# Optimization experiments

Hardware: AMD Instinct MI355X
Metric: run time of the kernel (lower is better)

Reference implementation:

```python
import jax, jax.numpy as jnp
import numpy as np

CH = 512
HEADS = 4
GROUPS = 32  # _groups(512) -> 32
EPS = 1e-5


def setup_inputs() -> dict:
    key = jax.random.key(0)
    ks = jax.random.split(key, 7)
    b, c, h, w = 16, CH, 32, 32
    sd = 1.0 / np.sqrt(c)
    return {
        "x": jax.random.normal(ks[0], (b, c, h, w), dtype=jnp.float32),
        "gamma": jnp.ones((c,), jnp.float32),
        "beta": jnp.zeros((c,), jnp.float32),
        "w_qkv": jax.random.normal(ks[1], (3 * c, c), dtype=jnp.float32) * sd,
        "b_qkv": jax.random.normal(ks[2], (3 * c,), dtype=jnp.float32) * 0.01,
        "w_proj": jax.random.normal(ks[3], (c, c), dtype=jnp.float32) * sd,
        "b_proj": jax.random.normal(ks[4], (c,), dtype=jnp.float32) * 0.01,
    }


def _group_norm(x, gamma, beta):
    b, c, h, w = x.shape
    xg = x.reshape(b, GROUPS, -1)  # (b, G, c//G * h * w)
    mu = jnp.mean(xg, axis=-1, keepdims=True)
    var = jnp.var(xg, axis=-1, keepdims=True)
    xn = ((xg - mu) * jax.lax.rsqrt(var + EPS)).reshape(b, c, h, w)
    return xn * gamma[None, :, None, None] + beta[None, :, None, None]


def reference(x, gamma, beta, w_qkv, b_qkv, w_proj, b_proj):
    b, c, h, w = x.shape
    hd = c // HEADS
    xn = _group_norm(x, gamma, beta)
    # 1x1 conv == channel matmul
    qkv = jnp.einsum('oc,bchw->bohw', w_qkv, xn) + b_qkv[None, :, None, None]
    qkv = qkv.reshape(b, 3, HEADS, hd, h * w)
    q, k, v = qkv[:, 0], qkv[:, 1], qkv[:, 2]  # (b, H, hd, n)
    scale = hd ** -0.5
    attn = jax.nn.softmax(jnp.einsum('bhcn,bhcm->bhnm', q * scale, k), axis=-1)
    out = jnp.einsum('bhnm,bhcm->bhcn', attn, v).reshape(b, c, h, w)
    out = jnp.einsum('oc,bchw->bohw', w_proj, out) + b_proj[None, :, None, None]
    return x + out
```

## Files before the change

### kernel.cpp

```cpp
#include <hip/hip_runtime.h>

#define CH 512
#define HEADS 4
#define HD 128
#define NPIX 1024
#define BATCH 16
#define GROUPS 32
#define GSZ 16
#define EPS 1e-5f

typedef _Float16 f16;
typedef _Float16 f16x8 __attribute__((ext_vector_type(8)));
typedef _Float16 f16x4 __attribute__((ext_vector_type(4)));
typedef float f32x4 __attribute__((ext_vector_type(4)));

__device__ __forceinline__ void gld16(const f16* g, f16* l) {
    __builtin_amdgcn_global_load_lds((__attribute__((address_space(1))) const void*)g,
                                     (__attribute__((address_space(3))) void*)l, 16, 0, 0);
}

__global__ __launch_bounds__(256, 2) void k_pre(const float* __restrict__ x, const float* __restrict__ gamma,
                                                const float* __restrict__ beta, f16* __restrict__ xnT,
                                                const float* __restrict__ wq, const float* __restrict__ wp,
                                                f16* __restrict__ wqT, f16* __restrict__ wpT) {
    __shared__ float xs[GSZ * NPIX];
    __shared__ float red[8];
    __shared__ float stat2[2];
    int bidx = blockIdx.x;
    if (bidx >= 512) {
        int c = (bidx - 512) * 256 + threadIdx.x;
        {
            int ot = c >> 13, kbl = (c >> 7) & 63, ol = c & 127;
            const float* s = wq + ((size_t)(ot * 128 + ol)) * CH + kbl * 8;
            f32x4 a = *(const f32x4*)s, b2 = *(const f32x4*)(s + 4);
            f16x8 v;
            v[0] = (f16)a.x; v[1] = (f16)a.y; v[2] = (f16)a.z; v[3] = (f16)a.w;
            v[4] = (f16)b2.x; v[5] = (f16)b2.y; v[6] = (f16)b2.z; v[7] = (f16)b2.w;
            *(f16x8*)(wqT + (size_t)c * 8) = v;
        }
        if (c < 32768) {
            int ot = c >> 13, kbl = (c >> 7) & 63, ol = c & 127;
            const float* s = wp + ((size_t)(ot * 128 + ol)) * CH + kbl * 8;
            f32x4 a = *(const f32x4*)s, b2 = *(const f32x4*)(s + 4);
            f16x8 v;
            v[0] = (f16)a.x; v[1] = (f16)a.y; v[2] = (f16)a.z; v[3] = (f16)a.w;
            v[4] = (f16)b2.x; v[5] = (f16)b2.y; v[6] = (f16)b2.z; v[7] = (f16)b2.w;
            *(f16x8*)(wpT + (size_t)c * 8) = v;
        }
        return;
    }
    int g = bidx & 31, b = bidx >> 5;
    const f32x4* x4 = (const f32x4*)(x + ((size_t)(b * GROUPS + g)) * (GSZ * NPIX));
    float s = 0.f, ss = 0.f;
    for (int i = threadIdx.x; i < GSZ * NPIX / 4; i += 256) {
        f32x4 v = x4[i];
        *(f32x4*)&xs[i * 4] = v;
        s  += v.x + v.y + v.z + v.w;
        ss += v.x * v.x + v.y * v.y + v.z * v.z + v.w * v.w;
    }
    for (int off = 32; off; off >>= 1) { s += __shfl_down(s, off); ss += __shfl_down(ss, off); }
    int wv = threadIdx.x >> 6, ln = threadIdx.x & 63;
    if (ln == 0) { red[wv] = s; red[4 + wv] = ss; }
    __syncthreads();
    if (threadIdx.x == 0) {
        float S = red[0] + red[1] + red[2] + red[3];
        float SS = red[4] + red[5] + red[6] + red[7];
        float mu = S / (GSZ * NPIX);
        float var = SS / (GSZ * NPIX) - mu * mu;
        stat2[0] = mu; stat2[1] = rsqrtf(var + EPS);
    }
    __syncthreads();
    float mu = stat2[0], rstd = stat2[1];
    int ch = threadIdx.x >> 7;
    int n  = threadIdx.x & 127;
    float gl[8], bl[8];
#pragma unroll
    for (int i = 0; i < 8; i++) {
        float gv = gamma[g * 16 + ch * 8 + i] * rstd;
        gl[i] = gv;
        bl[i] = beta[g * 16 + ch * 8 + i] - mu * gv;
    }
    f16* tb0 = xnT + ((size_t)(b * 8)) * 65536 + (g * 2 + ch) * 1024 + n * 8;
#pragma unroll
    for (int nt = 0; nt < 8; nt++) {
        f16x8 o;
#pragma unroll
        for (int i = 0; i < 8; i++)
            o[i] = (f16)(xs[(ch * 8 + i) * 1024 + nt * 128 + n] * gl[i] + bl[i]);
        *(f16x8*)(tb0 + (size_t)nt * 65536) = o;
    }
}

__global__ __launch_bounds__(256, 3) void k_qkv(const f16* __restrict__ wT, const float* __restrict__ bias,
                                                const f16* __restrict__ xnT, f16* __restrict__ qF,
                                                f16* __restrict__ kTl, f16* __restrict__ vTl) {
    int nt = blockIdx.x, ot = blockIdx.y, b = blockIdx.z;
    int o0 = ot * 128;
    __shared__ union SM {
        struct { f16 As[8192]; f16 Bs[8192]; } s;
        f16 Cf[16384];
    } sm;
    __shared__ float biasS[128];
    if (threadIdx.x < 128) biasS[threadIdx.x] = bias[o0 + threadIdx.x];
    int tid = threadIdx.x, lane = tid & 63, wv = tid >> 6;
    int wr = wv >> 1, wc = wv & 1;
    int l15 = lane & 15, quad = lane >> 4;
    const f16* wA = wT + (size_t)ot * 65536;
    const f16* xB = xnT + ((size_t)(b * 8 + nt)) * 65536;
    f32x4 acc[4][4] = {};
    for (int kk = 0; kk < CH; kk += 64) {
        __syncthreads();
        const f16* sa = wA + (size_t)(kk >> 3) * 1024;
        const f16* sb = xB + (size_t)(kk >> 3) * 1024;
#pragma unroll
        for (int i = 0; i < 4; i++) {
            int s = wv * 4 + i;
            gld16(sa + (size_t)(s * 64 + lane) * 8, sm.s.As + s * 512);
            gld16(sb + (size_t)(s * 64 + lane) * 8, sm.s.Bs + s * 512);
        }
        __syncthreads();
#pragma unroll
        for (int dk = 0; dk < 2; dk++) {
            f16x8 af[4], bf[4];
#pragma unroll
            for (int t = 0; t < 4; t++) {
                af[t] = *(const f16x8*)(sm.s.As + (dk * 4 + quad) * 1024 + (wr * 64 + t * 16 + l15) * 8);
                bf[t] = *(const f16x8*)(sm.s.Bs + (dk * 4 + quad) * 1024 + (wc * 64 + t * 16 + l15) * 8);
            }
#pragma unroll
            for (int tm = 0; tm < 4; tm++)
#pragma unroll
                for (int tn = 0; tn < 4; tn++)
                    acc[tm][tn] = __builtin_amdgcn_mfma_f32_16x16x32_f16(af[tm], bf[tn], acc[tm][tn], 0, 0, 0);
        }
    }
    __syncthreads();
    int which = ot >> 2, h = ot & 3;
#pragma unroll
    for (int tm = 0; tm < 4; tm++)
#pragma unroll
        for (int tn = 0; tn < 4; tn++) {
            int ob = wr * 64 + tm * 16 + quad * 4;
            int n  = wc * 64 + tn * 16 + l15;
            f16x4 pv;
#pragma unroll
            for (int r = 0; r < 4; r++) pv[r] = (f16)(acc[tm][tn][r] + biasS[ob + r]);
            if (which == 0) {
                int addr = ((((n >> 5) * 2 + ((n >> 4) & 1)) * 4 + (ob >> 5)) * 512)
                         + ((ob >> 3) & 3) * 128 + (n & 15) * 8 + (quad & 1) * 4;
                *(f16x4*)&sm.Cf[addr] = pv;
            } else if (which == 1) {
                int addr = (ob >> 3) * 1024 + n * 8 + (quad & 1) * 4;
                *(f16x4*)&sm.Cf[addr] = pv;
            } else {
#pragma unroll
                for (int r = 0; r < 4; r++)
                    sm.Cf[(n >> 3) * 1024 + (ob + r) * 8 + (n & 7)] = pv[r];
            }
        }
    __syncthreads();
    f16* tb = (which == 0) ? (qF + ((size_t)((b * 4 + h) * 8 + nt)) * 16384)
            : (which == 1) ? (kTl + ((size_t)((b * 4 + h) * 8 + nt)) * 16384)
                           : (vTl + ((size_t)((b * 4 + h) * 8 + nt)) * 16384);
#pragma unroll
    for (int i = 0; i < 8; i++) {
        int cid = tid + i * 256;
        *(f16x8*)(tb + (size_t)cid * 8) = *(const f16x8*)(sm.Cf + cid * 8);
    }
}

__global__ __launch_bounds__(512, 4) void k_attn(const f16* __restrict__ qF, const f16* __restrict__ kTl,
                                                 const f16* __restrict__ vTl, f16* __restrict__ oT) {
    __shared__ f16 smem[16384];
    f16* Kl = smem;
    f16* Vl = smem + 8192;
    int bid = blockIdx.x;
    int nt = bid >> 6, group = bid & 63;
    int b = group >> 2, h = group & 3;
    int tid = threadIdx.x, lane = tid & 63, wv = tid >> 6;
    int wq = wv & 3, role = wv >> 2;
    int l15 = lane & 15, quad = lane >> 4;
    const f16* qb = qF + ((size_t)(group * 8 + nt)) * 16384;
    const f16* kb = kTl + (size_t)group * 8 * 16384;
    const f16* vb = vTl + (size_t)group * 8 * 16384;
    f16* dstL = role ? Vl : Kl;

    f16x8 aq[4];
#pragma unroll
    for (int dk = 0; dk < 4; dk++) {
        f16x8 v = *(const f16x8*)(qb + (wv * 4 + dk) * 512 + lane * 8);
        aq[dk] = v * (f16)(0.08838834764831845f * 1.4426950408889634f);
    }

    float m_i = -1e30f, l_i = 0.f;
    f32x4 oaccT[8] = {};

    f16x8 buf[4];
    if (role == 0) {
#pragma unroll
        for (int i = 0; i < 4; i++)
            buf[i] = *(const f16x8*)(kb + (size_t)(wq * 4 + i) * 1024 + lane * 8);
    } else {
#pragma unroll
        for (int i = 0; i < 4; i++)
            buf[i] = *(const f16x8*)(vb + (size_t)(wq * 4 + i) * 512 + lane * 8);
    }

    for (int mc = 0; mc < 16; mc++) {
        __syncthreads();
#pragma unroll
        for (int i = 0; i < 4; i++)
            *(f16x8*)&dstL[(wq * 4 + i) * 512 + lane * 8] = buf[i];
        __syncthreads();

        f32x4 st[4] = {};
#pragma unroll
        for (int dk = 0; dk < 4; dk++) {
            f16x8 kf[4];
#pragma unroll
            for (int t = 0; t < 4; t++)
                kf[t] = *(const f16x8*)&Kl[(dk * 4 + quad) * 512 + (t * 16 + l15) * 8];
#pragma unroll
            for (int tc = 0; tc < 4; tc++)
                st[tc] = __builtin_amdgcn_mfma_f32_16x16x32_f16(kf[tc], aq[dk], st[tc], 0, 0, 0);
        }

        float a[4];
#pragma unroll
        for (int tc = 0; tc < 4; tc++)
            a[tc] = fmaxf(fmaxf(st[tc][0], st[tc][1]), fmaxf(st[tc][2], st[tc][3]));
        a[0] = fmaxf(a[0], a[2]); a[1] = fmaxf(a[1], a[3]);
        float mx = fmaxf(a[0], a[1]);
        mx = fmaxf(mx, __shfl_xor(mx, 16));
        mx = fmaxf(mx, __shfl_xor(mx, 32));

        bool full = !__all(mx <= m_i + 8.f);
        float mnew = m_i, alpha = 1.f;
        if (full) {
            mnew = fmaxf(m_i, mx);
            alpha = __builtin_amdgcn_exp2f(m_i - mnew);
            m_i = mnew;
        }

        float r4[4];
#pragma unroll
        for (int tc = 0; tc < 4; tc++) {
            float p0 = __builtin_amdgcn_exp2f(st[tc][0] - mnew);
            float p1 = __builtin_amdgcn_exp2f(st[tc][1] - mnew);
            float p2 = __builtin_amdgcn_exp2f(st[tc][2] - mnew);
            float p3 = __builtin_amdgcn_exp2f(st[tc][3] - mnew);
            st[tc][0] = p0; st[tc][1] = p1;
            st[tc][2] = p2; st[tc][3] = p3;
            r4[tc] = (p0 + p1) + (p2 + p3);
        }
        float rs = (r4[0] + r4[1]) + (r4[2] + r4[3]);
        rs += __shfl_xor(rs, 16);
        rs += __shfl_xor(rs, 32);
        if (full) {
            l_i = l_i * alpha + rs;
#pragma unroll
            for (int tc = 0; tc < 8; tc++) {
                oaccT[tc].x *= alpha; oaccT[tc].y *= alpha;
                oaccT[tc].z *= alpha; oaccT[tc].w *= alpha;
            }
        } else {
            l_i += rs;
        }

        f16x4 pf[4];
#pragma unroll
        for (int tc = 0; tc < 4; tc++)
#pragma unroll
            for (int r = 0; r < 4; r++) pf[tc][r] = (f16)st[tc][r];

        if (mc < 15) {
            if (role == 0) {
                const f16* s = kb + (size_t)((mc + 1) >> 1) * 16384 + (size_t)((mc + 1) & 1) * 512;
#pragma unroll
                for (int i = 0; i < 4; i++)
                    buf[i] = *(const f16x8*)(s + (size_t)(wq * 4 + i) * 1024 + lane * 8);
            } else {
                const f16* s = vb + (size_t)(mc + 1) * 8192;
#pragma unroll
                for (int i = 0; i < 4; i++)
                    buf[i] = *(const f16x8*)(s + (size_t)(wq * 4 + i) * 512 + lane * 8);
            }
        }

#pragma unroll
        for (int kblk = 0; kblk < 4; kblk++) {
#pragma unroll
            for (int t = 0; t < 8; t++) {
                f16x4 vf = *(const f16x4*)&Vl[(kblk * 2 + (quad >> 1)) * 1024 + (t * 16 + l15) * 8 + (quad & 1) * 4];
                oaccT[t] = __builtin_amdgcn_mfma_f32_16x16x16f16(vf, pf[kblk], oaccT[t], 0, 0, 0);
            }
        }
    }

    __syncthreads();
    {
        float inv = 1.f / l_i;
        int n = wv * 16 + l15;
#pragma unroll
        for (int tc = 0; tc < 8; tc++) {
            int blk = tc * 2 + (quad >> 1);
            f16x4 ov;
#pragma unroll
            for (int r = 0; r < 4; r++) ov[r] = (f16)(oaccT[tc][r] * inv);
            *(f16x4*)&smem[n * 128 + ((blk ^ (n & 15)) << 3) + ((quad & 1) << 2)] = ov;
        }
    }
    __syncthreads();
    f16* ob = oT + ((size_t)(b * 8 + nt)) * 65536;
#pragma unroll
    for (int i = 0; i < 4; i++) {
        int cid = tid + i * 512;
        int cbl = cid >> 7, n = cid & 127;
        f16x8 v = *(const f16x8*)&smem[n * 128 + ((cbl ^ (n & 15)) << 3)];
        *(f16x8*)(ob + (size_t)(h * 16 + cbl) * 1024 + n * 8) = v;
    }
}

__global__ __launch_bounds__(256, 3) void k_proj(const f16* __restrict__ wT, const float* __restrict__ bias,
                                                 const f16* __restrict__ oT, const float* __restrict__ x,
                                                 float* __restrict__ out) {
    int nt = blockIdx.x, ot = blockIdx.y, b = blockIdx.z;
    int n0 = nt * 128, o0 = ot * 128;
    __shared__ union SM {
        struct { f16 As[8192]; f16 Bs[8192]; } s;
        f16 Cs[128][136];
    } sm;
    __shared__ float biasS[128];
    if (threadIdx.x < 128) biasS[threadIdx.x] = bias[o0 + threadIdx.x];
    int tid = threadIdx.x, lane = tid & 63, wv = tid >> 6;
    int wr = wv >> 1, wc = wv & 1;
    int l15 = lane & 15, quad = lane >> 4;
    const f16* wA = wT + (size_t)ot * 65536;
    const f16* xB = oT + ((size_t)(b * 8 + nt)) * 65536;
    f32x4 acc[4][4] = {};
    for (int kk = 0; kk < CH; kk += 64) {
        __syncthreads();
        const f16* sa = wA + (size_t)(kk >> 3) * 1024;
        const f16* sb = xB + (size_t)(kk >> 3) * 1024;
#pragma unroll
        for (int i = 0; i < 4; i++) {
            int s = wv * 4 + i;
            gld16(sa + (size_t)(s * 64 + lane) * 8, sm.s.As + s * 512);
            gld16(sb + (size_t)(s * 64 + lane) * 8, sm.s.Bs + s * 512);
        }
        __syncthreads();
#pragma unroll
        for (int dk = 0; dk < 2; dk++) {
            f16x8 af[4], bf[4];
#pragma unroll
            for (int t = 0; t < 4; t++) {
                af[t] = *(const f16x8*)(sm.s.As + (dk * 4 + quad) * 1024 + (wr * 64 + t * 16 + l15) * 8);
                bf[t] = *(const f16x8*)(sm.s.Bs + (dk * 4 + quad) * 1024 + (wc * 64 + t * 16 + l15) * 8);
            }
#pragma unroll
            for (int tm = 0; tm < 4; tm++)
#pragma unroll
                for (int tn = 0; tn < 4; tn++)
                    acc[tm][tn] = __builtin_amdgcn_mfma_f32_16x16x32_f16(af[tm], bf[tn], acc[tm][tn], 0, 0, 0);
        }
    }
    __syncthreads();
#pragma unroll
    for (int tm = 0; tm < 4; tm++)
#pragma unroll
        for (int tn = 0; tn < 4; tn++)
#pragma unroll
            for (int r = 0; r < 4; r++) {
                int o = wr * 64 + tm * 16 + quad * 4 + r;
                int n = wc * 64 + tn * 16 + l15;
                sm.Cs[o][n] = (f16)(acc[tm][tn][r] + biasS[o]);
            }
    __syncthreads();
#pragma unroll
    for (int i = 0; i < 8; i++) {
        int cid = tid + i * 256;
        int row = cid >> 4, off = (cid & 15) * 8;
        f16x8 v = *(const f16x8*)&sm.Cs[row][off];
        size_t gofs = ((size_t)(b * CH) + o0 + row) * NPIX + n0 + off;
        const float* xp = x + gofs;
        float* op = out + gofs;
        f32x4 o0v, o1v;
        o0v.x = xp[0] + (float)v[0]; o0v.y = xp[1] + (float)v[1];
        o0v.z = xp[2] + (float)v[2]; o0v.w = xp[3] + (float)v[3];
        o1v.x = xp[4] + (float)v[4]; o1v.y = xp[5] + (float)v[5];
        o1v.z = xp[6] + (float)v[6]; o1v.w = xp[7] + (float)v[7];
        *(f32x4*)op = o0v; *(f32x4*)(op + 4) = o1v;
    }
}

extern "C" void kernel_launch(void* const* d_in, const int* in_sizes, int n_in,
                              void* d_out, int out_size, void* d_ws, size_t ws_size,
                              hipStream_t stream) {
    const float* x     = (const float*)d_in[0];
    const float* gamma = (const float*)d_in[1];
    const float* beta  = (const float*)d_in[2];
    const float* wqkv  = (const float*)d_in[3];
    const float* bqkv  = (const float*)d_in[4];
    const float* wproj = (const float*)d_in[5];
    const float* bproj = (const float*)d_in[6];
    float* out = (float*)d_out;

    char* p = (char*)d_ws;
    f16* wqT = (f16*)p;           p += (size_t)3 * CH * CH * 2;
    f16* wpT = (f16*)p;           p += (size_t)CH * CH * 2;
    f16* xnT = (f16*)p;           p += (size_t)BATCH * NPIX * CH * 2;
    f16* qF  = (f16*)p;           p += (size_t)BATCH * HEADS * NPIX * HD * 2;
    f16* kTl = (f16*)p;           p += (size_t)BATCH * HEADS * NPIX * HD * 2;
    f16* vTl = (f16*)p;           p += (size_t)BATCH * HEADS * NPIX * HD * 2;
    f16* oT  = (f16*)p;           p += (size_t)BATCH * NPIX * CH * 2;

    k_pre<<<dim3(896), 256, 0, stream>>>(x, gamma, beta, xnT, wqkv, wproj, wqT, wpT);
    k_qkv<<<dim3(8, 12, BATCH), 256, 0, stream>>>(wqT, bqkv, xnT, qF, kTl, vTl);
    k_attn<<<dim3(512), 512, 0, stream>>>(qF, kTl, vTl, oT);
    k_proj<<<dim3(8, 4, BATCH), 256, 0, stream>>>(wpT, bproj, oT, x, out);
}
```

Before: 221.3 us.

## Process two query tiles per wave in attention and stage P through LDS

The attention kernel now runs with 256 threads per block, and each wave handles two 16-row query tiles. Each K/V fragment read from LDS therefore feeds two MFMAs, which halves LDS traffic per FLOP. The P matrix is written to a per-wave swizzled LDS buffer so the PV product can use the wider 16x16x32 MFMA instead of 16x16x16. In exchange, each thread holds more registers, the kernel uses more LDS, and the launch bound drops to 3 blocks with fewer waves per block, which lowers occupancy and latency hiding.

```diff
diff --git a/kernel.cpp b/kernel.cpp
--- a/kernel.cpp
+++ b/kernel.cpp
@@ -169,51 +169,56 @@
     }
 }
 
-__global__ __launch_bounds__(512, 4) void k_attn(const f16* __restrict__ qF, const f16* __restrict__ kTl,
+__global__ __launch_bounds__(256, 3) void k_attn(const f16* __restrict__ qF, const f16* __restrict__ kTl,
                                                  const f16* __restrict__ vTl, f16* __restrict__ oT) {
-    __shared__ f16 smem[16384];
+    __shared__ f16 smem[24576];
     f16* Kl = smem;
     f16* Vl = smem + 8192;
     int bid = blockIdx.x;
     int nt = bid >> 6, group = bid & 63;
     int b = group >> 2, h = group & 3;
     int tid = threadIdx.x, lane = tid & 63, wv = tid >> 6;
-    int wq = wv & 3, role = wv >> 2;
     int l15 = lane & 15, quad = lane >> 4;
     const f16* qb = qF + ((size_t)(group * 8 + nt)) * 16384;
     const f16* kb = kTl + (size_t)group * 8 * 16384;
     const f16* vb = vTl + (size_t)group * 8 * 16384;
-    f16* dstL = role ? Vl : Kl;
-
-    f16x8 aq[4];
-#pragma unroll
-    for (int dk = 0; dk < 4; dk++) {
-        f16x8 v = *(const f16x8*)(qb + (wv * 4 + dk) * 512 + lane * 8);
-        aq[dk] = v * (f16)(0.08838834764831845f * 1.4426950408889634f);
-    }
-
-    float m_i = -1e30f, l_i = 0.f;
-    f32x4 oaccT[8] = {};
-
-    f16x8 buf[4];
-    if (role == 0) {
-#pragma unroll
-        for (int i = 0; i < 4; i++)
-            buf[i] = *(const f16x8*)(kb + (size_t)(wq * 4 + i) * 1024 + lane * 8);
+    f16* Pw = smem + 16384 + wv * 2048;
+
+    int srow = (wv & 1) * 8;
+    bool stageK = (wv < 2);
+    f16* dstL = stageK ? Kl : Vl;
+
+    f16x8 aq[2][4];
+#pragma unroll
+    for (int u = 0; u < 2; u++)
+#pragma unroll
+        for (int dk = 0; dk < 4; dk++) {
+            f16x8 v = *(const f16x8*)(qb + ((wv * 2 + u) * 4 + dk) * 512 + lane * 8);
+            aq[u][dk] = v * (f16)(0.08838834764831845f * 1.4426950408889634f);
+        }
+
+    float m_i[2] = {-1e30f, -1e30f}, l_i[2] = {0.f, 0.f};
+    f32x4 oacc[2][8] = {};
+
+    f16x8 buf[8];
+    if (stageK) {
+#pragma unroll
+        for (int i = 0; i < 8; i++)
+            buf[i] = *(const f16x8*)(kb + (size_t)(srow + i) * 1024 + lane * 8);
     } else {
 #pragma unroll
-        for (int i = 0; i < 4; i++)
-            buf[i] = *(const f16x8*)(vb + (size_t)(wq * 4 + i) * 512 + lane * 8);
+        for (int i = 0; i < 8; i++)
+            buf[i] = *(const f16x8*)(vb + (size_t)(srow + i) * 512 + lane * 8);
     }
 
     for (int mc = 0; mc < 16; mc++) {
         __syncthreads();
 #pragma unroll
-        for (int i = 0; i < 4; i++)
-            *(f16x8*)&dstL[(wq * 4 + i) * 512 + lane * 8] = buf[i];
-        __syncthreads();
-
-        f32x4 st[4] = {};
+        for (int i = 0; i < 8; i++)
+            *(f16x8*)&dstL[(srow + i) * 512 + lane * 8] = buf[i];
+        __syncthreads();
+
+        f32x4 st[2][4] = {};
 #pragma unroll
         for (int dk = 0; dk < 4; dk++) {
             f16x8 kf[4];
@@ -221,100 +226,112 @@
             for (int t = 0; t < 4; t++)
                 kf[t] = *(const f16x8*)&Kl[(dk * 4 + quad) * 512 + (t * 16 + l15) * 8];
 #pragma unroll
+            for (int tc = 0; tc < 4; tc++) {
+                st[0][tc] = __builtin_amdgcn_mfma_f32_16x16x32_f16(kf[tc], aq[0][dk], st[0][tc], 0, 0, 0);
+                st[1][tc] = __builtin_amdgcn_mfma_f32_16x16x32_f16(kf[tc], aq[1][dk], st[1][tc], 0, 0, 0);
+            }
+        }
+
+#pragma unroll
+        for (int u = 0; u < 2; u++) {
+            float a[4];
+#pragma unroll
             for (int tc = 0; tc < 4; tc++)
-                st[tc] = __builtin_amdgcn_mfma_f32_16x16x32_f16(kf[tc], aq[dk], st[tc], 0, 0, 0);
-        }
-
-        float a[4];
-#pragma unroll
-        for (int tc = 0; tc < 4; tc++)
-            a[tc] = fmaxf(fmaxf(st[tc][0], st[tc][1]), fmaxf(st[tc][2], st[tc][3]));
-        a[0] = fmaxf(a[0], a[2]); a[1] = fmaxf(a[1], a[3]);
-        float mx = fmaxf(a[0], a[1]);
-        mx = fmaxf(mx, __shfl_xor(mx, 16));
-        mx = fmaxf(mx, __shfl_xor(mx, 32));
-
-        bool full = !__all(mx <= m_i + 8.f);
-        float mnew = m_i, alpha = 1.f;
-        if (full) {
-            mnew = fmaxf(m_i, mx);
-            alpha = __builtin_amdgcn_exp2f(m_i - mnew);
-            m_i = mnew;
-        }
-
-        float r4[4];
-#pragma unroll
-        for (int tc = 0; tc < 4; tc++) {
-            float p0 = __builtin_amdgcn_exp2f(st[tc][0] - mnew);
-            float p1 = __builtin_amdgcn_exp2f(st[tc][1] - mnew);
-            float p2 = __builtin_amdgcn_exp2f(st[tc][2] - mnew);
-            float p3 = __builtin_amdgcn_exp2f(st[tc][3] - mnew);
-            st[tc][0] = p0; st[tc][1] = p1;
-            st[tc][2] = p2; st[tc][3] = p3;
-            r4[tc] = (p0 + p1) + (p2 + p3);
-        }
-        float rs = (r4[0] + r4[1]) + (r4[2] + r4[3]);
-        rs += __shfl_xor(rs, 16);
-        rs += __shfl_xor(rs, 32);
-        if (full) {
-            l_i = l_i * alpha + rs;
-#pragma unroll
-            for (int tc = 0; tc < 8; tc++) {
-                oaccT[tc].x *= alpha; oaccT[tc].y *= alpha;
-                oaccT[tc].z *= alpha; oaccT[tc].w *= alpha;
-            }
-        } else {
-            l_i += rs;
-        }
-
-        f16x4 pf[4];
-#pragma unroll
-        for (int tc = 0; tc < 4; tc++)
-#pragma unroll
-            for (int r = 0; r < 4; r++) pf[tc][r] = (f16)st[tc][r];
+                a[tc] = fmaxf(fmaxf(st[u][tc][0], st[u][tc][1]), fmaxf(st[u][tc][2], st[u][tc][3]));
+            a[0] = fmaxf(a[0], a[2]); a[1] = fmaxf(a[1], a[3]);
+            float mx = fmaxf(a[0], a[1]);
+            mx = fmaxf(mx, __shfl_xor(mx, 16));
+            mx = fmaxf(mx, __shfl_xor(mx, 32));
+
+            bool full = !__all(mx <= m_i[u] + 8.f);
+            float mnew = m_i[u], alpha = 1.f;
+            if (full) {
+                mnew = fmaxf(m_i[u], mx);
+                alpha = __builtin_amdgcn_exp2f(m_i[u] - mnew);
+                m_i[u] = mnew;
+            }
+
+            float r4[4];
+#pragma unroll
+            for (int tc = 0; tc < 4; tc++) {
+                float p0 = __builtin_amdgcn_exp2f(st[u][tc][0] - mnew);
+                float p1 = __builtin_amdgcn_exp2f(st[u][tc][1] - mnew);
+                float p2 = __builtin_amdgcn_exp2f(st[u][tc][2] - mnew);
+                float p3 = __builtin_amdgcn_exp2f(st[u][tc][3] - mnew);
+                st[u][tc][0] = p0; st[u][tc][1] = p1;
+                st[u][tc][2] = p2; st[u][tc][3] = p3;
+                r4[tc] = (p0 + p1) + (p2 + p3);
+            }
+            float rs = (r4[0] + r4[1]) + (r4[2] + r4[3]);
+            rs += __shfl_xor(rs, 16);
+            rs += __shfl_xor(rs, 32);
+            if (full) {
+                l_i[u] = l_i[u] * alpha + rs;
+#pragma unroll
+                for (int tc = 0; tc < 8; tc++) {
+                    oacc[u][tc].x *= alpha; oacc[u][tc].y *= alpha;
+                    oacc[u][tc].z *= alpha; oacc[u][tc].w *= alpha;
+                }
+            } else {
+                l_i[u] += rs;
+            }
+
+#pragma unroll
+            for (int tc = 0; tc < 4; tc++) {
+                int blk = tc * 2 + (quad >> 1);
+                f16x4 pv;
+#pragma unroll
+                for (int r = 0; r < 4; r++) pv[r] = (f16)st[u][tc][r];
+                *(f16x4*)&Pw[(u * 16 + l15) * 64 + ((blk ^ (l15 & 7)) << 3) + ((quad & 1) << 2)] = pv;
+            }
+        }
 
         if (mc < 15) {
-            if (role == 0) {
+            if (stageK) {
                 const f16* s = kb + (size_t)((mc + 1) >> 1) * 16384 + (size_t)((mc + 1) & 1) * 512;
 #pragma unroll
-                for (int i = 0; i < 4; i++)
-                    buf[i] = *(const f16x8*)(s + (size_t)(wq * 4 + i) * 1024 + lane * 8);
+                for (int i = 0; i < 8; i++)
+                    buf[i] = *(const f16x8*)(s + (size_t)(srow + i) * 1024 + lane * 8);
             } else {
                 const f16* s = vb + (size_t)(mc + 1) * 8192;
 #pragma unroll
-                for (int i = 0; i < 4; i++)
-                    buf[i] = *(const f16x8*)(s + (size_t)(wq * 4 + i) * 512 + lane * 8);
-            }
-        }
-
-#pragma unroll
-        for (int kblk = 0; kblk < 4; kblk++) {
+                for (int i = 0; i < 8; i++)
+                    buf[i] = *(const f16x8*)(s + (size_t)(srow + i) * 512 + lane * 8);
+            }
+        }
+
+#pragma unroll
+        for (int mk = 0; mk < 2; mk++) {
+            f16x8 pf0 = *(const f16x8*)&Pw[l15 * 64 + (((mk * 4 + quad) ^ (l15 & 7)) << 3)];
+            f16x8 pf1 = *(const f16x8*)&Pw[(16 + l15) * 64 + (((mk * 4 + quad) ^ (l15 & 7)) << 3)];
 #pragma unroll
             for (int t = 0; t < 8; t++) {
-                f16x4 vf = *(const f16x4*)&Vl[(kblk * 2 + (quad >> 1)) * 1024 + (t * 16 + l15) * 8 + (quad & 1) * 4];
-                oaccT[t] = __builtin_amdgcn_mfma_f32_16x16x16f16(vf, pf[kblk], oaccT[t], 0, 0, 0);
-            }
-        }
-    }
-
-    __syncthreads();
-    {
-        float inv = 1.f / l_i;
-        int n = wv * 16 + l15;
+                f16x8 vf = *(const f16x8*)&Vl[(mk * 4 + quad) * 1024 + (t * 16 + l15) * 8];
+                oacc[0][t] = __builtin_amdgcn_mfma_f32_16x16x32_f16(vf, pf0, oacc[0][t], 0, 0, 0);
+                oacc[1][t] = __builtin_amdgcn_mfma_f32_16x16x32_f16(vf, pf1, oacc[1][t], 0, 0, 0);
+            }
+        }
+    }
+
+    __syncthreads();
+#pragma unroll
+    for (int u = 0; u < 2; u++) {
+        float inv = 1.f / l_i[u];
+        int n = wv * 32 + u * 16 + l15;
 #pragma unroll
         for (int tc = 0; tc < 8; tc++) {
             int blk = tc * 2 + (quad >> 1);
             f16x4 ov;
 #pragma unroll
-            for (int r = 0; r < 4; r++) ov[r] = (f16)(oaccT[tc][r] * inv);
+            for (int r = 0; r < 4; r++) ov[r] = (f16)(oacc[u][tc][r] * inv);
             *(f16x4*)&smem[n * 128 + ((blk ^ (n & 15)) << 3) + ((quad & 1) << 2)] = ov;
         }
     }
     __syncthreads();
     f16* ob = oT + ((size_t)(b * 8 + nt)) * 65536;
 #pragma unroll
-    for (int i = 0; i < 4; i++) {
-        int cid = tid + i * 512;
+    for (int i = 0; i < 8; i++) {
+        int cid = tid + i * 256;
         int cbl = cid >> 7, n = cid & 127;
         f16x8 v = *(const f16x8*)&smem[n * 128 + ((cbl ^ (n & 15)) << 3)];
         *(f16x8*)(ob + (size_t)(h * 16 + cbl) * 1024 + n * 8) = v;
@@ -416,6 +433,6 @@
 
     k_pre<<<dim3(896), 256, 0, stream>>>(x, gamma, beta, xnT, wqkv, wproj, wqT, wpT);
     k_qkv<<<dim3(8, 12, BATCH), 256, 0, stream>>>(wqT, bqkv, xnT, qF, kTl, vTl);
-    k_attn<<<dim3(512), 512, 0, stream>>>(qF, kTl, vTl, oT);
+    k_attn<<<dim3(512), 256, 0, stream>>>(qF, kTl, vTl, oT);
     k_proj<<<dim3(8, 4, BATCH), 256, 0, stream>>>(wpT, bproj, oT, x, out);
 }
```

After: 244.3 us. +10.4%, slower.

## Rework attention kernel around 32x32 MFMA tiles with double-buffered async K/V staging

Applied to the files above, without the earlier changes.

The attention kernel moves from 512 threads using 16x16 MFMAs to 256 threads, each wave owning 32 query rows and using 32x32x16 MFMAs for both QK^T and PV. K/V tiles are now double-buffered in dynamic shared memory (80KB) and filled with direct global-to-LDS loads, replacing the register-staged copy and one barrier per iteration. The P matrix goes through a swizzled per-wave LDS scratch to reach the B-operand layout. Per-wave register pressure and LDS use go up, which can lower occupancy, and a shared-memory attribute call is added on every launch.

```diff
diff --git a/kernel.cpp b/kernel.cpp
--- a/kernel.cpp
+++ b/kernel.cpp
@@ -13,6 +13,7 @@
 typedef _Float16 f16x8 __attribute__((ext_vector_type(8)));
 typedef _Float16 f16x4 __attribute__((ext_vector_type(4)));
 typedef float f32x4 __attribute__((ext_vector_type(4)));
+typedef float f32x16 __attribute__((ext_vector_type(16)));
 
 __device__ __forceinline__ void gld16(const f16* g, f16* l) {
     __builtin_amdgcn_global_load_lds((__attribute__((address_space(1))) const void*)g,
@@ -169,69 +170,71 @@
     }
 }
 
-__global__ __launch_bounds__(512, 4) void k_attn(const f16* __restrict__ qF, const f16* __restrict__ kTl,
+__global__ __launch_bounds__(256, 2) void k_attn(const f16* __restrict__ qF, const f16* __restrict__ kTl,
                                                  const f16* __restrict__ vTl, f16* __restrict__ oT) {
-    __shared__ f16 smem[16384];
-    f16* Kl = smem;
-    f16* Vl = smem + 8192;
+    extern __shared__ f16 smem[];
     int bid = blockIdx.x;
     int nt = bid >> 6, group = bid & 63;
     int b = group >> 2, h = group & 3;
     int tid = threadIdx.x, lane = tid & 63, wv = tid >> 6;
-    int wq = wv & 3, role = wv >> 2;
-    int l15 = lane & 15, quad = lane >> 4;
+    int l31 = lane & 31, halfl = lane >> 5;
     const f16* qb = qF + ((size_t)(group * 8 + nt)) * 16384;
     const f16* kb = kTl + (size_t)group * 8 * 16384;
     const f16* vb = vTl + (size_t)group * 8 * 16384;
-    f16* dstL = role ? Vl : Kl;
-
-    f16x8 aq[4];
-#pragma unroll
-    for (int dk = 0; dk < 4; dk++) {
-        f16x8 v = *(const f16x8*)(qb + (wv * 4 + dk) * 512 + lane * 8);
-        aq[dk] = v * (f16)(0.08838834764831845f * 1.4426950408889634f);
+    f16* Pw = smem + 32768 + wv * 2048;
+
+    f16x8 aq[8];
+    {
+        int bq = (wv * 2 + ((lane >> 4) & 1)) * 4;
+#pragma unroll
+        for (int s = 0; s < 8; s++) {
+            f16x8 v = *(const f16x8*)(qb + (bq + (s >> 1)) * 512 + ((s & 1) * 2 + halfl) * 128 + (lane & 15) * 8);
+            aq[s] = v * (f16)(0.08838834764831845f * 1.4426950408889634f);
+        }
     }
 
     float m_i = -1e30f, l_i = 0.f;
-    f32x4 oaccT[8] = {};
-
-    f16x8 buf[4];
-    if (role == 0) {
-#pragma unroll
-        for (int i = 0; i < 4; i++)
-            buf[i] = *(const f16x8*)(kb + (size_t)(wq * 4 + i) * 1024 + lane * 8);
-    } else {
-#pragma unroll
-        for (int i = 0; i < 4; i++)
-            buf[i] = *(const f16x8*)(vb + (size_t)(wq * 4 + i) * 512 + lane * 8);
-    }
+    f32x16 oacc[4] = {};
+
+    auto stage = [&](int mc, f16* dst) {
+        if (wv < 2) {
+            const f16* src = kb + (size_t)(mc >> 1) * 16384 + (size_t)(mc & 1) * 512;
+#pragma unroll
+            for (int i = 0; i < 8; i++)
+                gld16(src + (size_t)(wv * 8 + i) * 1024 + lane * 8, dst + (wv * 8 + i) * 512);
+        } else {
+            const f16* src = vb + (size_t)mc * 8192;
+#pragma unroll
+            for (int i = 0; i < 8; i++)
+                gld16(src + (size_t)((wv - 2) * 8 + i) * 512 + lane * 8, dst + 8192 + ((wv - 2) * 8 + i) * 512);
+        }
+    };
+
+    stage(0, smem);
 
     for (int mc = 0; mc < 16; mc++) {
         __syncthreads();
-#pragma unroll
-        for (int i = 0; i < 4; i++)
-            *(f16x8*)&dstL[(wq * 4 + i) * 512 + lane * 8] = buf[i];
-        __syncthreads();
-
-        f32x4 st[4] = {};
-#pragma unroll
-        for (int dk = 0; dk < 4; dk++) {
-            f16x8 kf[4];
-#pragma unroll
-            for (int t = 0; t < 4; t++)
-                kf[t] = *(const f16x8*)&Kl[(dk * 4 + quad) * 512 + (t * 16 + l15) * 8];
-#pragma unroll
-            for (int tc = 0; tc < 4; tc++)
-                st[tc] = __builtin_amdgcn_mfma_f32_16x16x32_f16(kf[tc], aq[dk], st[tc], 0, 0, 0);
-        }
-
-        float a[4];
-#pragma unroll
-        for (int tc = 0; tc < 4; tc++)
-            a[tc] = fmaxf(fmaxf(st[tc][0], st[tc][1]), fmaxf(st[tc][2], st[tc][3]));
-        a[0] = fmaxf(a[0], a[2]); a[1] = fmaxf(a[1], a[3]);
-        float mx = fmaxf(a[0], a[1]);
-        mx = fmaxf(mx, __shfl_xor(mx, 16));
+        f16* Kc = smem + (mc & 1) * 16384;
+        f16* Vc = Kc + 8192;
+        if (mc < 15) stage(mc + 1, smem + ((mc + 1) & 1) * 16384);
+
+        f32x16 st0 = {}, st1 = {};
+#pragma unroll
+        for (int s = 0; s < 8; s++) {
+            f16x8 k0 = *(const f16x8*)&Kc[(s * 2 + halfl) * 512 + l31 * 8];
+            f16x8 k1 = *(const f16x8*)&Kc[(s * 2 + halfl) * 512 + (32 + l31) * 8];
+            st0 = __builtin_amdgcn_mfma_f32_32x32x16_f16(k0, aq[s], st0, 0, 0, 0);
+            st1 = __builtin_amdgcn_mfma_f32_32x32x16_f16(k1, aq[s], st1, 0, 0, 0);
+        }
+
+        float a[16];
+#pragma unroll
+        for (int i = 0; i < 16; i++) a[i] = fmaxf(st0[i], st1[i]);
+#pragma unroll
+        for (int i = 0; i < 8; i++) a[i] = fmaxf(a[i], a[i + 8]);
+#pragma unroll
+        for (int i = 0; i < 4; i++) a[i] = fmaxf(a[i], a[i + 4]);
+        float mx = fmaxf(fmaxf(a[0], a[1]), fmaxf(a[2], a[3]));
         mx = fmaxf(mx, __shfl_xor(mx, 32));
 
         bool full = !__all(mx <= m_i + 8.f);
@@ -242,57 +245,46 @@
             m_i = mnew;
         }
 
-        float r4[4];
-#pragma unroll
-        for (int tc = 0; tc < 4; tc++) {
-            float p0 = __builtin_amdgcn_exp2f(st[tc][0] - mnew);
-            float p1 = __builtin_amdgcn_exp2f(st[tc][1] - mnew);
-            float p2 = __builtin_amdgcn_exp2f(st[tc][2] - mnew);
-            float p3 = __builtin_amdgcn_exp2f(st[tc][3] - mnew);
-            st[tc][0] = p0; st[tc][1] = p1;
-            st[tc][2] = p2; st[tc][3] = p3;
-            r4[tc] = (p0 + p1) + (p2 + p3);
-        }
-        float rs = (r4[0] + r4[1]) + (r4[2] + r4[3]);
-        rs += __shfl_xor(rs, 16);
+        float r[16];
+#pragma unroll
+        for (int i = 0; i < 16; i++) {
+            float p0 = __builtin_amdgcn_exp2f(st0[i] - mnew);
+            float p1 = __builtin_amdgcn_exp2f(st1[i] - mnew);
+            st0[i] = p0; st1[i] = p1;
+            r[i] = p0 + p1;
+        }
+#pragma unroll
+        for (int i = 0; i < 8; i++) r[i] += r[i + 8];
+#pragma unroll
+        for (int i = 0; i < 4; i++) r[i] += r[i + 4];
+        float rs = (r[0] + r[1]) + (r[2] + r[3]);
         rs += __shfl_xor(rs, 32);
         if (full) {
             l_i = l_i * alpha + rs;
 #pragma unroll
-            for (int tc = 0; tc < 8; tc++) {
-                oaccT[tc].x *= alpha; oaccT[tc].y *= alpha;
-                oaccT[tc].z *= alpha; oaccT[tc].w *= alpha;
-            }
+            for (int dt = 0; dt < 4; dt++)
+#pragma unroll
+                for (int i = 0; i < 16; i++) oacc[dt][i] *= alpha;
         } else {
             l_i += rs;
         }
 
-        f16x4 pf[4];
-#pragma unroll
-        for (int tc = 0; tc < 4; tc++)
-#pragma unroll
-            for (int r = 0; r < 4; r++) pf[tc][r] = (f16)st[tc][r];
-
-        if (mc < 15) {
-            if (role == 0) {
-                const f16* s = kb + (size_t)((mc + 1) >> 1) * 16384 + (size_t)((mc + 1) & 1) * 512;
-#pragma unroll
-                for (int i = 0; i < 4; i++)
-                    buf[i] = *(const f16x8*)(s + (size_t)(wq * 4 + i) * 1024 + lane * 8);
-            } else {
-                const f16* s = vb + (size_t)(mc + 1) * 8192;
-#pragma unroll
-                for (int i = 0; i < 4; i++)
-                    buf[i] = *(const f16x8*)(s + (size_t)(wq * 4 + i) * 512 + lane * 8);
-            }
-        }
-
-#pragma unroll
-        for (int kblk = 0; kblk < 4; kblk++) {
-#pragma unroll
-            for (int t = 0; t < 8; t++) {
-                f16x4 vf = *(const f16x4*)&Vl[(kblk * 2 + (quad >> 1)) * 1024 + (t * 16 + l15) * 8 + (quad & 1) * 4];
-                oaccT[t] = __builtin_amdgcn_mfma_f32_16x16x16f16(vf, pf[kblk], oaccT[t], 0, 0, 0);
+#pragma unroll
+        for (int g = 0; g < 4; g++) {
+            f16x4 pv0, pv1;
+#pragma unroll
+            for (int rr = 0; rr < 4; rr++) { pv0[rr] = (f16)st0[g * 4 + rr]; pv1[rr] = (f16)st1[g * 4 + rr]; }
+            *(f16x4*)&Pw[l31 * 64 + ((g ^ (l31 & 7)) << 3) + (halfl << 2)] = pv0;
+            *(f16x4*)&Pw[l31 * 64 + (((4 + g) ^ (l31 & 7)) << 3) + (halfl << 2)] = pv1;
+        }
+
+#pragma unroll
+        for (int ks = 0; ks < 4; ks++) {
+            f16x8 pf = *(const f16x8*)&Pw[l31 * 64 + (((ks * 2 + halfl) ^ (l31 & 7)) << 3)];
+#pragma unroll
+            for (int dt = 0; dt < 4; dt++) {
+                f16x8 vf = *(const f16x8*)&Vc[(ks * 2 + halfl) * 1024 + (dt * 32 + l31) * 8];
+                oacc[dt] = __builtin_amdgcn_mfma_f32_32x32x16_f16(vf, pf, oacc[dt], 0, 0, 0);
             }
         }
     }
@@ -300,21 +292,23 @@
     __syncthreads();
     {
         float inv = 1.f / l_i;
-        int n = wv * 16 + l15;
-#pragma unroll
-        for (int tc = 0; tc < 8; tc++) {
-            int blk = tc * 2 + (quad >> 1);
-            f16x4 ov;
-#pragma unroll
-            for (int r = 0; r < 4; r++) ov[r] = (f16)(oaccT[tc][r] * inv);
-            *(f16x4*)&smem[n * 128 + ((blk ^ (n & 15)) << 3) + ((quad & 1) << 2)] = ov;
-        }
+        int n = wv * 32 + l31;
+#pragma unroll
+        for (int dt = 0; dt < 4; dt++)
+#pragma unroll
+            for (int g = 0; g < 4; g++) {
+                f16x4 ov;
+#pragma unroll
+                for (int rr = 0; rr < 4; rr++) ov[rr] = (f16)(oacc[dt][g * 4 + rr] * inv);
+                int cbl = dt * 4 + g;
+                *(f16x4*)&smem[n * 128 + ((cbl ^ (n & 15)) << 3) + (halfl << 2)] = ov;
+            }
     }
     __syncthreads();
     f16* ob = oT + ((size_t)(b * 8 + nt)) * 65536;
 #pragma unroll
-    for (int i = 0; i < 4; i++) {
-        int cid = tid + i * 512;
+    for (int i = 0; i < 8; i++) {
+        int cid = tid + i * 256;
         int cbl = cid >> 7, n = cid & 127;
         f16x8 v = *(const f16x8*)&smem[n * 128 + ((cbl ^ (n & 15)) << 3)];
         *(f16x8*)(ob + (size_t)(h * 16 + cbl) * 1024 + n * 8) = v;
@@ -416,6 +410,9 @@
 
     k_pre<<<dim3(896), 256, 0, stream>>>(x, gamma, beta, xnT, wqkv, wproj, wqT, wpT);
     k_qkv<<<dim3(8, 12, BATCH), 256, 0, stream>>>(wqT, bqkv, xnT, qF, kTl, vTl);
-    k_attn<<<dim3(512), 512, 0, stream>>>(qF, kTl, vTl, oT);
+
+    hipFuncSetAttribute((const void*)k_attn, hipFuncAttributeMaxDynamicSharedMemorySize, 81920);
+    k_attn<<<dim3(512), 256, 81920, stream>>>(qF, kTl, vTl, oT);
+
     k_proj<<<dim3(8, 4, BATCH), 256, 0, stream>>>(wpT, bproj, oT, x, out);
 }
```

New measurement: 201.2 us (median of 2 runs). -9.1%, faster.
